# Kernel tuning notes

Measured on AMD Instinct MI355X. Metric: run time of the kernel, lower is better.

## Reference

```python
import jax, jax.numpy as jnp
import numpy as np

EMBED = 1024
HEADS = 16
HEAD_DIM = EMBED // HEADS


def setup_inputs() -> dict:
    key = jax.random.key(0)
    ks = jax.random.split(key, 8)
    b, t, d = 2, 2048, EMBED
    s = 1.0 / np.sqrt(d)
    return {
        'k': jax.random.normal(ks[0], (b, t, d), jnp.float32),
        'q': jax.random.normal(ks[1], (b, t, d), jnp.float32),
        'v': jax.random.normal(ks[2], (b, t, d), jnp.float32),
        'Wk': jax.random.normal(ks[3], (d, d), jnp.float32) * s,
        'Wq': jax.random.normal(ks[4], (d, d), jnp.float32) * s,
        'Wv': jax.random.normal(ks[5], (d, d), jnp.float32) * s,
        'Wo': jax.random.normal(ks[6], (d, d), jnp.float32) * s,
        'bo': jax.random.normal(ks[7], (d,), jnp.float32) * 0.01,
    }


def reference(k, q, v, Wk, Wq, Wv, Wo, bo):
    b, t, d = q.shape
    h, n = HEADS, HEAD_DIM
    # projections (q_prj bias=False, k/v bias=False per add_bias_kv=False)
    keys = (k @ Wk.T).reshape(b, t, h, n).transpose(0, 2, 1, 3)      # b h t n
    queries = (q @ Wq.T).reshape(b, t, h, n).transpose(0, 2, 1, 3)
    values = (v @ Wv.T).reshape(b, t, h, n).transpose(0, 2, 1, 3)
    att = jnp.einsum('bhtn,bhsn->bhts', queries, keys)               # b h t t
    att = jax.nn.softmax(att / np.sqrt(n), axis=-1)
    out = jnp.einsum('bhts,bhsn->bhtn', att, values)                 # b h t n
    out = out.transpose(0, 2, 1, 3).reshape(b, t, d)                 # b t (h n)
    return out @ Wo.T + bo
```

## Files before the change

### kernel.cpp

```cpp
#include <hip/hip_runtime.h>
#include <hip/hip_bf16.h>


typedef unsigned short u16;
typedef unsigned int   u32;
using short8 = __attribute__((ext_vector_type(8))) short;
using f32x4  = __attribute__((ext_vector_type(4))) float;

__device__ __forceinline__ u16 f2b(float f) {
    u32 u = __float_as_uint(f);
    u += 0x7FFFu + ((u >> 16) & 1u);
    return (u16)(u >> 16);
}
__device__ __forceinline__ u32 pack2(float lo, float hi) {
    union { __hip_bfloat162 h; u32 u; } c;
    c.h = __float22bfloat162_rn(make_float2(lo, hi));
    return c.u;
}
__device__ __forceinline__ float fexp2(float x) {
    return __builtin_amdgcn_exp2f(x);
}
__device__ __forceinline__ void gld_lds16(const u16* g, u16* l) {
    __builtin_amdgcn_global_load_lds(
        (const __attribute__((address_space(1))) void*)g,
        (__attribute__((address_space(3))) void*)l, 16, 0, 0);
}

__global__ __launch_bounds__(256) void convert_kernel(
    const float* s0, const float* s1, const float* s2, const float* s3,
    const float* s4, const float* s5, const float* s6,
    u16* d0, u16* d1, u16* d2, u16* d3, u16* d4, u16* d5, u16* d6)
{
    const int y = blockIdx.y;
    const float* s; u16* d; u32 n;
    switch (y) {
        case 0: s = s0; d = d0; n = 1048576; break;
        case 1: s = s1; d = d1; n = 1048576; break;
        case 2: s = s2; d = d2; n = 1048576; break;
        case 3: s = s3; d = d3; n = 262144; break;
        case 4: s = s4; d = d4; n = 262144; break;
        case 5: s = s5; d = d5; n = 262144; break;
        default: s = s6; d = d6; n = 262144; break;
    }
    for (u32 i = blockIdx.x * 256 + threadIdx.x; i < n; i += 256 * 1024) {
        float4 f = ((const float4*)s)[i];
        uint2 o; o.x = pack2(f.x, f.y); o.y = pack2(f.z, f.w);
        ((uint2*)d)[i] = o;
    }
}

template <int MODE>
__device__ __forceinline__ void gemm_core(
    const u16* __restrict__ A, const u16* __restrict__ B,
    void* __restrict__ C, const float* __restrict__ bias, float scale,
    u32 bm, u32 bn)
{
    constexpr u32 K = 1024;
    __shared__ u16 As[128 * 32];
    __shared__ u16 Bs[128 * 32];

    const int tid  = threadIdx.x;
    const int lane = tid & 63;
    const int w    = tid >> 6;
    const int wr   = w >> 1, wc = w & 1;
    const int ml   = lane & 15, g = lane >> 4;

    f32x4 acc[4][4] = {};

    const u32 srow = w * 32 + (lane >> 2);
    const u32 scol = (u32)(((lane & 3) ^ ((lane >> 3) & 3)) * 8);
    const u16* gA = A + (size_t)(bm + srow) * K + scol;
    const u16* gB = B + (size_t)(bn + srow) * K + scol;
    u16* lA = &As[w * 1024];
    u16* lB = &Bs[w * 1024];

    const u32 fsw = (u32)((g ^ ((ml >> 1) & 3)) * 8);

    for (u32 k0 = 0; k0 < K; k0 += 32) {
        __syncthreads();
        gld_lds16(gA + k0, lA);
        gld_lds16(gA + 16 * K + k0, lA + 512);
        gld_lds16(gB + k0, lB);
        gld_lds16(gB + 16 * K + k0, lB + 512);
        __syncthreads();

        short8 af[4], bf[4];
#pragma unroll
        for (int it = 0; it < 4; ++it)
            af[it] = *(const short8*)&As[(wr * 64 + it * 16 + ml) * 32 + fsw];
#pragma unroll
        for (int ct = 0; ct < 4; ++ct)
            bf[ct] = *(const short8*)&Bs[(wc * 64 + ct * 16 + ml) * 32 + fsw];
#pragma unroll
        for (int it = 0; it < 4; ++it)
#pragma unroll
            for (int ct = 0; ct < 4; ++ct)
                acc[it][ct] = __builtin_amdgcn_mfma_f32_16x16x32_bf16(
                    af[it], bf[ct], acc[it][ct], 0, 0, 0);
    }

    if (MODE == 3) {
#pragma unroll
        for (int ct = 0; ct < 4; ++ct) {
            const u32 col = bn + wc * 64 + ct * 16 + ml;
            u16* dst = (u16*)C + (col >> 11) * 2097152 + (col & 2047);
#pragma unroll
            for (int it = 0; it < 4; ++it) {
                const u32 row = bm + wr * 64 + it * 16 + g * 4;
#pragma unroll
                for (int r = 0; r < 4; ++r)
                    dst[(size_t)(row + r) * 2048] = f2b(acc[it][ct][r]);
            }
        }
    } else {
#pragma unroll
        for (int ct = 0; ct < 4; ++ct) {
            const u32 col = bn + wc * 64 + ct * 16 + ml;
            const float bv = (MODE == 2 && bias) ? bias[col] : 0.0f;
#pragma unroll
            for (int it = 0; it < 4; ++it) {
                const u32 row = bm + wr * 64 + it * 16 + g * 4;
#pragma unroll
                for (int r = 0; r < 4; ++r) {
                    const float v = acc[it][ct][r] * scale + bv;
                    if (MODE == 2) ((float*)C)[(size_t)(row + r) * 1024 + col] = v;
                    else           ((u16*)C)[(size_t)(row + r) * 1024 + col] = f2b(v);
                }
            }
        }
    }
}

__global__ __launch_bounds__(256) void proj3_kernel(
    const u16* kb, const u16* qb, const u16* vb,
    const u16* Wkb, const u16* Wqb, const u16* Wvb,
    u16* Kp, u16* Qp, u16* Vt)
{
    if (blockIdx.z == 0)
        gemm_core<0>(kb, Wkb, Kp, nullptr, 1.0f, blockIdx.y * 128, blockIdx.x * 128);
    else if (blockIdx.z == 1)
        gemm_core<0>(qb, Wqb, Qp, nullptr, 0.18033688011112042f, blockIdx.y * 128, blockIdx.x * 128);
    else
        gemm_core<3>(Wvb, vb, Vt, nullptr, 1.0f, blockIdx.x * 128, blockIdx.y * 128);
}

__global__ __launch_bounds__(256) void out_gemm_kernel(
    const u16* __restrict__ A, const u16* __restrict__ W,
    float* __restrict__ C, const float* __restrict__ bias)
{
    constexpr u32 K = 1024;
    __shared__ u16 As[64 * 32];
    __shared__ u16 Bs[128 * 32];

    const int tid  = threadIdx.x;
    const int lane = tid & 63;
    const int w    = tid >> 6;
    const int wr   = w >> 1, wc = w & 1;
    const int ml   = lane & 15, g = lane >> 4;
    const u32 bm   = blockIdx.y * 64, bn = blockIdx.x * 128;

    f32x4 acc[2][4] = {};

    const u32 scol = (u32)(((lane & 3) ^ ((lane >> 3) & 3)) * 8);
    const u16* gA = A + (size_t)(bm + w * 16 + (lane >> 2)) * K + scol;
    const u16* gB = W + (size_t)(bn + w * 32 + (lane >> 2)) * K + scol;
    u16* lA = &As[w * 512];
    u16* lB = &Bs[w * 1024];

    const u32 fsw = (u32)((g ^ ((ml >> 1) & 3)) * 8);

    for (u32 k0 = 0; k0 < K; k0 += 32) {
        __syncthreads();
        gld_lds16(gA + k0, lA);
        gld_lds16(gB + k0, lB);
        gld_lds16(gB + 16 * K + k0, lB + 512);
        __syncthreads();

        short8 af[2], bf[4];
#pragma unroll
        for (int it = 0; it < 2; ++it)
            af[it] = *(const short8*)&As[(wr * 32 + it * 16 + ml) * 32 + fsw];
#pragma unroll
        for (int ct = 0; ct < 4; ++ct)
            bf[ct] = *(const short8*)&Bs[(wc * 64 + ct * 16 + ml) * 32 + fsw];
#pragma unroll
        for (int it = 0; it < 2; ++it)
#pragma unroll
            for (int ct = 0; ct < 4; ++ct)
                acc[it][ct] = __builtin_amdgcn_mfma_f32_16x16x32_bf16(
                    af[it], bf[ct], acc[it][ct], 0, 0, 0);
    }

#pragma unroll
    for (int ct = 0; ct < 4; ++ct) {
        const u32 col = bn + wc * 64 + ct * 16 + ml;
        const float bv = bias ? bias[col] : 0.0f;
#pragma unroll
        for (int it = 0; it < 2; ++it) {
            const u32 row = bm + wr * 32 + it * 16 + g * 4;
#pragma unroll
            for (int r = 0; r < 4; ++r)
                C[(size_t)(row + r) * 1024 + col] = acc[it][ct][r] + bv;
        }
    }
}

__global__ __launch_bounds__(512, 4) void attn_kernel(
    const u16* __restrict__ Qp, const u16* __restrict__ Kp,
    const u16* __restrict__ Vt, u16* __restrict__ Op)
{
    __shared__ u16   Ks[2 * 4096];
    __shared__ u16   Vs[2 * 4096];
    __shared__ u16   Ps[8 * 1280];
    __shared__ float Ls[4][32];

    const int tid  = threadIdx.x;
    const int lane = tid & 63;
    const int w    = tid >> 6;
    const int wq   = w >> 1;
    const int ws   = w & 1;
    const int ml   = lane & 15;
    const int g    = lane >> 4;

    const u32 fid  = blockIdx.x + (blockIdx.y << 4);
    const u32 swz  = (fid & 7) * 64 + (fid >> 3);
    const u32 bh   = swz >> 4;
    const u32 t0   = (swz & 15) * 128;
    const u32 b    = bh >> 4, h = bh & 15;

    const u32 base  = b * 2048 * 1024 + h * 64;
    const u32 vbase = bh * 64 * 2048;

    short8 bq[2][2];
#pragma unroll
    for (int qt = 0; qt < 2; ++qt) {
        const u16* qr = Qp + base + (t0 + wq * 32 + qt * 16 + ml) * 1024 + g * 8;
        bq[qt][0] = *(const short8*)qr;
        bq[qt][1] = *(const short8*)(qr + 32);
    }

    f32x4 oacc[4][2] = {};
    float l4[2] = {};

    const u32 srow = (u32)(lane >> 3);
    const u32 schk = (u32)((lane & 7) ^ (lane >> 3));
    const u16* gK = Kp + base + (size_t)(w * 8 + srow) * 1024 + schk * 8;
    const u16* gV = Vt + vbase + (size_t)(w * 8 + srow) * 2048 + schk * 8;
    u16* lK0 = &Ks[w * 512];
    u16* lK1 = &Ks[4096 + w * 512];
    u16* lV0 = &Vs[w * 512];
    u16* lV1 = &Vs[4096 + w * 512];

    const u32 kaOff = (u32)((ws * 32 + ml) * 64 + ((g ^ (ml & 7)) * 8));
    const u32 vaOff = (u32)(ml * 64 + (((ws * 4 + g) ^ (ml & 7)) * 8));
    u16* Pw  = &Ps[w * 1280];
    u32* PwU = (u32*)Pw;
    const u32 pWr = (u32)(ml * 20 + g * 2);
    const u32 pRd = (u32)(ml * 40 + g * 8);

#define ATTN_STAGE(KD, VD)                                                   \
    { gld_lds16(gK, (KD)); gld_lds16(gV, (VD)); gK += 65536; gV += 64; }

#define ATTN_COMPUTE(KB, VB)                                                 \
    {                                                                        \
        short8 vv[4];                                                        \
        _Pragma("unroll")                                                    \
        for (int dt = 0; dt < 4; ++dt)                                       \
            vv[dt] = *(const short8*)&(VB)[vaOff + dt * 1024];               \
        _Pragma("unroll")                                                    \
        for (int sub = 0; sub < 2; ++sub) {                                  \
            short8 k0 = *(const short8*)&(KB)[kaOff + sub * 1024];           \
            short8 k1 = *(const short8*)&(KB)[(kaOff ^ 32) + sub * 1024];    \
            _Pragma("unroll")                                                \
            for (int qt = 0; qt < 2; ++qt) {                                 \
                f32x4 z = {};                                                \
                z = __builtin_amdgcn_mfma_f32_16x16x32_bf16(                 \
                    k0, bq[qt][0], z, 0, 0, 0);                              \
                z = __builtin_amdgcn_mfma_f32_16x16x32_bf16(                 \
                    k1, bq[qt][1], z, 0, 0, 0);                              \
                const float p0 = fexp2(z[0]), p1 = fexp2(z[1]);              \
                const float p2 = fexp2(z[2]), p3 = fexp2(z[3]);              \
                l4[qt] += (p0 + p1) + (p2 + p3);                             \
                uint2 pv; pv.x = pack2(p0, p1); pv.y = pack2(p2, p3);        \
                *(uint2*)&PwU[pWr + (u32)(qt * 320 + sub * 8)] = pv;         \
            }                                                                \
        }                                                                    \
        _Pragma("unroll")                                                    \
        for (int qt = 0; qt < 2; ++qt) {                                     \
            short8 pb = *(const short8*)&Pw[pRd + (u32)(qt * 640)];          \
            _Pragma("unroll")                                                \
            for (int dt = 0; dt < 4; ++dt)                                   \
                oacc[dt][qt] = __builtin_amdgcn_mfma_f32_16x16x32_bf16(      \
                    vv[dt], pb, oacc[dt][qt], 0, 0, 0);                      \
        }                                                                    \
    }

    ATTN_STAGE(lK0, lV0)
    __syncthreads();

#pragma unroll 1
    for (int it = 0; it < 16; ++it) {
        ATTN_STAGE(lK1, lV1)
        ATTN_COMPUTE(Ks, Vs)
        __syncthreads();
        if (it < 15) ATTN_STAGE(lK0, lV0)
        ATTN_COMPUTE(Ks + 4096, Vs + 4096)
        __syncthreads();
    }
#undef ATTN_STAGE
#undef ATTN_COMPUTE

#pragma unroll
    for (int qt = 0; qt < 2; ++qt) {
        l4[qt] += __shfl_xor(l4[qt], 16);
        l4[qt] += __shfl_xor(l4[qt], 32);
    }

    float* Rw = (wq < 2) ? ((float*)Ks + wq * 2048) : ((float*)Vs + (wq - 2) * 2048);
    if (ws == 1) {
#pragma unroll
        for (int dt = 0; dt < 4; ++dt)
#pragma unroll
            for (int qt = 0; qt < 2; ++qt)
#pragma unroll
                for (int r = 0; r < 4; ++r)
                    Rw[(dt * 16 + g * 4 + r) * 32 + qt * 16 + ml] = oacc[dt][qt][r];
        if (g == 0) {
#pragma unroll
            for (int qt = 0; qt < 2; ++qt) Ls[wq][qt * 16 + ml] = l4[qt];
        }
    }
    __syncthreads();
    if (ws == 0) {
#pragma unroll
        for (int dt = 0; dt < 4; ++dt)
#pragma unroll
            for (int qt = 0; qt < 2; ++qt)
#pragma unroll
                for (int r = 0; r < 4; ++r)
                    oacc[dt][qt][r] += Rw[(dt * 16 + g * 4 + r) * 32 + qt * 16 + ml];
#pragma unroll
        for (int qt = 0; qt < 2; ++qt) {
            const u32 q = (u32)(wq * 32 + qt * 16 + ml);
            const float inv = 1.0f / (l4[qt] + Ls[wq][qt * 16 + ml]);
            const u32 row = (b * 2048 + t0 + q) * 1024 + h * 64;
#pragma unroll
            for (int dt = 0; dt < 4; ++dt) {
                const u32 ci = row + dt * 16 + g * 4;
                *(u32*)&Op[ci]     = pack2(oacc[dt][qt][0] * inv, oacc[dt][qt][1] * inv);
                *(u32*)&Op[ci + 2] = pack2(oacc[dt][qt][2] * inv, oacc[dt][qt][3] * inv);
            }
        }
    }
}

extern "C" void kernel_launch(void* const* d_in, const int* in_sizes, int n_in,
                              void* d_out, int out_size, void* d_ws, size_t ws_size,
                              hipStream_t stream)
{
    const float* kin = (const float*)d_in[0];
    const float* qin = (const float*)d_in[1];
    const float* vin = (const float*)d_in[2];
    const float* Wk  = (const float*)d_in[3];
    const float* Wq  = (const float*)d_in[4];
    const float* Wv  = (const float*)d_in[5];
    const float* Wo  = (const float*)d_in[6];
    const float* bo  = (const float*)d_in[7];
    float* out = (float*)d_out;

    const size_t ACT = 4194304;
    const size_t WSZ = 1048576;

    u16* kb  = (u16*)d_ws;
    u16* qb  = kb + ACT;
    u16* vb  = qb + ACT;
    u16* Wkb = vb + ACT;
    u16* Wqb = Wkb + WSZ;
    u16* Wvb = Wqb + WSZ;
    u16* Wob = Wvb + WSZ;
    u16* Kp  = Wob + WSZ;
    u16* Qp  = Kp + ACT;
    u16* Vt  = Qp + ACT;
    u16* Op  = kb;

    convert_kernel<<<dim3(1024, 7), 256, 0, stream>>>(
        kin, qin, vin, Wk, Wq, Wv, Wo, kb, qb, vb, Wkb, Wqb, Wvb, Wob);
    proj3_kernel<<<dim3(8, 32, 3), 256, 0, stream>>>(
        kb, qb, vb, Wkb, Wqb, Wvb, Kp, Qp, Vt);
    attn_kernel<<<dim3(16, 32), 512, 0, stream>>>(Qp, Kp, Vt, Op);
    out_gemm_kernel<<<dim3(8, 64), 256, 0, stream>>>(Op, Wob, out, bo);
}
```

Baseline: 211.9 us.

## Double-buffer LDS in projection and output GEMMs and swizzle block order

Both GEMM kernels now keep two LDS buffers and issue the global-to-LDS load for the next K slice before computing on the current one. This drops one barrier per step and overlaps load latency with MFMA work. Block indices are also remapped so consecutive blocks share A/B rows, which should improve L2 reuse. The cost is double the LDS per block, which can lower occupancy.

```diff
diff --git a/kernel.cpp b/kernel.cpp
--- a/kernel.cpp
+++ b/kernel.cpp
@@ -56,8 +56,8 @@
     u32 bm, u32 bn)
 {
     constexpr u32 K = 1024;
-    __shared__ u16 As[128 * 32];
-    __shared__ u16 Bs[128 * 32];
+    __shared__ u16 As[2 * 128 * 32];
+    __shared__ u16 Bs[2 * 128 * 32];
 
     const int tid  = threadIdx.x;
     const int lane = tid & 63;
@@ -71,33 +71,49 @@
     const u32 scol = (u32)(((lane & 3) ^ ((lane >> 3) & 3)) * 8);
     const u16* gA = A + (size_t)(bm + srow) * K + scol;
     const u16* gB = B + (size_t)(bn + srow) * K + scol;
-    u16* lA = &As[w * 1024];
-    u16* lB = &Bs[w * 1024];
+    u16* lA0 = &As[w * 1024];
+    u16* lB0 = &Bs[w * 1024];
+    u16* lA1 = lA0 + 4096;
+    u16* lB1 = lB0 + 4096;
 
     const u32 fsw = (u32)((g ^ ((ml >> 1) & 3)) * 8);
 
-    for (u32 k0 = 0; k0 < K; k0 += 32) {
-        __syncthreads();
-        gld_lds16(gA + k0, lA);
-        gld_lds16(gA + 16 * K + k0, lA + 512);
-        gld_lds16(gB + k0, lB);
-        gld_lds16(gB + 16 * K + k0, lB + 512);
-        __syncthreads();
-
-        short8 af[4], bf[4];
-#pragma unroll
-        for (int it = 0; it < 4; ++it)
-            af[it] = *(const short8*)&As[(wr * 64 + it * 16 + ml) * 32 + fsw];
-#pragma unroll
-        for (int ct = 0; ct < 4; ++ct)
-            bf[ct] = *(const short8*)&Bs[(wc * 64 + ct * 16 + ml) * 32 + fsw];
-#pragma unroll
-        for (int it = 0; it < 4; ++it)
-#pragma unroll
-            for (int ct = 0; ct < 4; ++ct)
-                acc[it][ct] = __builtin_amdgcn_mfma_f32_16x16x32_bf16(
-                    af[it], bf[ct], acc[it][ct], 0, 0, 0);
-    }
+#define G_STAGE(k0, la, lb)                                                  \
+    { gld_lds16(gA + (k0), (la));                                            \
+      gld_lds16(gA + 16 * K + (k0), (la) + 512);                             \
+      gld_lds16(gB + (k0), (lb));                                            \
+      gld_lds16(gB + 16 * K + (k0), (lb) + 512); }
+
+#define G_COMPUTE(AB, BB)                                                    \
+    {                                                                        \
+        short8 af[4], bf[4];                                                 \
+        _Pragma("unroll")                                                    \
+        for (int it2 = 0; it2 < 4; ++it2)                                    \
+            af[it2] = *(const short8*)&(AB)[(wr * 64 + it2 * 16 + ml) * 32 + fsw]; \
+        _Pragma("unroll")                                                    \
+        for (int ct = 0; ct < 4; ++ct)                                       \
+            bf[ct] = *(const short8*)&(BB)[(wc * 64 + ct * 16 + ml) * 32 + fsw]; \
+        _Pragma("unroll")                                                    \
+        for (int it2 = 0; it2 < 4; ++it2)                                    \
+            _Pragma("unroll")                                                \
+            for (int ct = 0; ct < 4; ++ct)                                   \
+                acc[it2][ct] = __builtin_amdgcn_mfma_f32_16x16x32_bf16(      \
+                    af[it2], bf[ct], acc[it2][ct], 0, 0, 0);                 \
+    }
+
+    G_STAGE(0, lA0, lB0)
+    __syncthreads();
+#pragma unroll 1
+    for (u32 it = 0; it < 16; ++it) {
+        G_STAGE(it * 64 + 32, lA1, lB1)
+        G_COMPUTE(As, Bs)
+        __syncthreads();
+        if (it < 15) G_STAGE(it * 64 + 64, lA0, lB0)
+        G_COMPUTE(As + 4096, Bs + 4096)
+        __syncthreads();
+    }
+#undef G_STAGE
+#undef G_COMPUTE
 
     if (MODE == 3) {
 #pragma unroll
@@ -136,12 +152,17 @@
     const u16* Wkb, const u16* Wqb, const u16* Wvb,
     u16* Kp, u16* Qp, u16* Vt)
 {
+    const u32 fid2 = blockIdx.x + (blockIdx.y << 3);
+    const u32 c    = fid2 & 7, i = fid2 >> 3;
+    const u32 by   = c * 4 + (i >> 3);
+    const u32 bx   = i & 7;
+
     if (blockIdx.z == 0)
-        gemm_core<0>(kb, Wkb, Kp, nullptr, 1.0f, blockIdx.y * 128, blockIdx.x * 128);
+        gemm_core<0>(kb, Wkb, Kp, nullptr, 1.0f, by * 128, bx * 128);
     else if (blockIdx.z == 1)
-        gemm_core<0>(qb, Wqb, Qp, nullptr, 0.18033688011112042f, blockIdx.y * 128, blockIdx.x * 128);
+        gemm_core<0>(qb, Wqb, Qp, nullptr, 0.18033688011112042f, by * 128, bx * 128);
     else
-        gemm_core<3>(Wvb, vb, Vt, nullptr, 1.0f, blockIdx.x * 128, blockIdx.y * 128);
+        gemm_core<3>(Wvb, vb, Vt, nullptr, 1.0f, bx * 128, by * 128);
 }
 
 __global__ __launch_bounds__(256) void out_gemm_kernel(
@@ -149,47 +170,68 @@
     float* __restrict__ C, const float* __restrict__ bias)
 {
     constexpr u32 K = 1024;
-    __shared__ u16 As[64 * 32];
-    __shared__ u16 Bs[128 * 32];
+    __shared__ u16 As[2 * 64 * 32];
+    __shared__ u16 Bs[2 * 128 * 32];
 
     const int tid  = threadIdx.x;
     const int lane = tid & 63;
     const int w    = tid >> 6;
     const int wr   = w >> 1, wc = w & 1;
     const int ml   = lane & 15, g = lane >> 4;
-    const u32 bm   = blockIdx.y * 64, bn = blockIdx.x * 128;
+
+    const u32 fid  = blockIdx.x + (blockIdx.y << 3);
+    const u32 c    = fid & 7, i = fid >> 3;
+    const u32 by   = c * 8 + (i >> 3);
+    const u32 bx   = i & 7;
+    const u32 bm   = by * 64, bn = bx * 128;
 
     f32x4 acc[2][4] = {};
 
     const u32 scol = (u32)(((lane & 3) ^ ((lane >> 3) & 3)) * 8);
     const u16* gA = A + (size_t)(bm + w * 16 + (lane >> 2)) * K + scol;
     const u16* gB = W + (size_t)(bn + w * 32 + (lane >> 2)) * K + scol;
-    u16* lA = &As[w * 512];
-    u16* lB = &Bs[w * 1024];
+    u16* lA0 = &As[w * 512];
+    u16* lB0 = &Bs[w * 1024];
+    u16* lA1 = lA0 + 2048;
+    u16* lB1 = lB0 + 4096;
 
     const u32 fsw = (u32)((g ^ ((ml >> 1) & 3)) * 8);
 
-    for (u32 k0 = 0; k0 < K; k0 += 32) {
-        __syncthreads();
-        gld_lds16(gA + k0, lA);
-        gld_lds16(gB + k0, lB);
-        gld_lds16(gB + 16 * K + k0, lB + 512);
-        __syncthreads();
-
-        short8 af[2], bf[4];
-#pragma unroll
-        for (int it = 0; it < 2; ++it)
-            af[it] = *(const short8*)&As[(wr * 32 + it * 16 + ml) * 32 + fsw];
-#pragma unroll
-        for (int ct = 0; ct < 4; ++ct)
-            bf[ct] = *(const short8*)&Bs[(wc * 64 + ct * 16 + ml) * 32 + fsw];
-#pragma unroll
-        for (int it = 0; it < 2; ++it)
-#pragma unroll
-            for (int ct = 0; ct < 4; ++ct)
-                acc[it][ct] = __builtin_amdgcn_mfma_f32_16x16x32_bf16(
-                    af[it], bf[ct], acc[it][ct], 0, 0, 0);
-    }
+#define G_STAGE(k0, la, lb)                                                  \
+    { gld_lds16(gA + (k0), (la));                                            \
+      gld_lds16(gB + (k0), (lb));                                            \
+      gld_lds16(gB + 16 * K + (k0), (lb) + 512); }
+
+#define G_COMPUTE(AB, BB)                                                    \
+    {                                                                        \
+        short8 af[2], bf[4];                                                 \
+        _Pragma("unroll")                                                    \
+        for (int it2 = 0; it2 < 2; ++it2)                                    \
+            af[it2] = *(const short8*)&(AB)[(wr * 32 + it2 * 16 + ml) * 32 + fsw]; \
+        _Pragma("unroll")                                                    \
+        for (int ct = 0; ct < 4; ++ct)                                       \
+            bf[ct] = *(const short8*)&(BB)[(wc * 64 + ct * 16 + ml) * 32 + fsw]; \
+        _Pragma("unroll")                                                    \
+        for (int it2 = 0; it2 < 2; ++it2)                                    \
+            _Pragma("unroll")                                                \
+            for (int ct = 0; ct < 4; ++ct)                                   \
+                acc[it2][ct] = __builtin_amdgcn_mfma_f32_16x16x32_bf16(      \
+                    af[it2], bf[ct], acc[it2][ct], 0, 0, 0);                 \
+    }
+
+    G_STAGE(0, lA0, lB0)
+    __syncthreads();
+#pragma unroll 1
+    for (u32 it = 0; it < 16; ++it) {
+        G_STAGE(it * 64 + 32, lA1, lB1)
+        G_COMPUTE(As, Bs)
+        __syncthreads();
+        if (it < 15) G_STAGE(it * 64 + 64, lA0, lB0)
+        G_COMPUTE(As + 2048, Bs + 4096)
+        __syncthreads();
+    }
+#undef G_STAGE
+#undef G_COMPUTE
 
 #pragma unroll
     for (int ct = 0; ct < 4; ++ct) {
```

After: 223.3 us. 5.4% more time.
